# Kernel optimization log

Measured on AMD Instinct MI355X. Metric: run time of the kernel, lower is better.

## Reference

```python
import jax, jax.numpy as jnp
import numpy as np

EPS = 1e-5
K = 9
DILATION = 1

def bn(x, g, b, m, v):
    # x: (B,C,N,1), inference-mode BatchNorm2d with running stats
    sh = (1, -1, 1, 1)
    return (x - m.reshape(sh)) * (g.reshape(sh) / jnp.sqrt(v.reshape(sh) + EPS)) + b.reshape(sh)

def conv1x1(x, w, b):
    # w: (Cout, Cin), x: (B,Cin,N,1)
    return jnp.einsum('oc,bcnj->bonj', w, x) + b.reshape(1, -1, 1, 1)

def knn_idx(feat, k):
    # feat: (B,C,N) -> (B,N,k) indices of k nearest nodes (incl. self)
    xt = jnp.transpose(feat, (0, 2, 1))  # (B,N,C)
    x2 = jnp.sum(xt * xt, axis=-1)       # (B,N)
    dist = x2[:, :, None] - 2.0 * jnp.einsum('bnc,bmc->bnm', xt, xt) + x2[:, None, :]
    _, idx = jax.lax.top_k(-dist, k)
    return idx

def setup_inputs():
    key = jax.random.key(0)
    ks = jax.random.split(key, 24)
    B, C, H, W = 16, 256, 32, 32
    HID = 512
    def g(i, shape, s=1.0):
        return jax.random.normal(ks[i], shape, dtype=jnp.float32) * s
    def pos(i, shape):
        return jax.random.uniform(ks[i], shape, dtype=jnp.float32, minval=0.5, maxval=1.5)
    return {
        'x': g(0, (B, C, H, W)),
        'fc1_w': g(1, (C, C), 0.05), 'fc1_b': g(2, (C,), 0.05),
        'bn1_g': pos(3, (C,)), 'bn1_b': g(4, (C,), 0.1), 'bn1_m': g(5, (C,), 0.1), 'bn1_v': pos(6, (C,)),
        'gc_w': g(7, (HID, 2 * C), 0.05), 'gc_b': g(8, (HID,), 0.05),
        'gbn_g': pos(9, (HID,)), 'gbn_b': g(10, (HID,), 0.1), 'gbn_m': g(11, (HID,), 0.1), 'gbn_v': pos(12, (HID,)),
        'bn2_g': pos(13, (HID,)), 'bn2_b': g(14, (HID,), 0.1), 'bn2_m': g(15, (HID,), 0.1), 'bn2_v': pos(16, (HID,)),
        'fc2_w': g(17, (C, HID), 0.05), 'fc2_b': g(18, (C,), 0.05),
        'bn3_g': pos(19, (C,)), 'bn3_b': g(20, (C,), 0.1), 'bn3_m': g(21, (C,), 0.1), 'bn3_v': pos(22, (C,)),
    }

def reference(x, fc1_w, fc1_b, bn1_g, bn1_b, bn1_m, bn1_v,
              gc_w, gc_b, gbn_g, gbn_b, gbn_m, gbn_v,
              bn2_g, bn2_b, bn2_m, bn2_v,
              fc2_w, fc2_b, bn3_g, bn3_b, bn3_m, bn3_v):
    B, C, H, W = x.shape
    N = H * W
    x = x.reshape(B, C, N, 1)
    shortcut = x
    # fc1: 1x1 conv + BN
    h = bn(conv1x1(x, fc1_w, fc1_b), bn1_g, bn1_b, bn1_m, bn1_v)
    # DyGraphConv2d: dynamic dilated kNN graph over N nodes
    feat = h[..., 0]  # (B,C,N)
    idx = knn_idx(feat, K * DILATION)[:, :, ::DILATION]  # (B,N,K)
    # MRConv2d: max over neighbors of (x_j - x_i)
    x_j = jax.vmap(lambda f, i: f[:, i])(feat, idx)        # (B,C,N,K) gather
    diff_max = jnp.max(x_j - feat[:, :, :, None], axis=-1)  # (B,C,N)
    # interleave [x, max_diff] along channel dim -> (B, 2C, N, 1)
    m = jnp.stack([feat, diff_max], axis=2).reshape(B, 2 * C, N, 1)
    g = conv1x1(m, gc_w, gc_b)
    g = bn(g, gbn_g, gbn_b, gbn_m, gbn_v)  # BasicConv BN, act='None'
    # graph_conv Sequential: BN + GELU (erf, torch default)
    g = jax.nn.gelu(bn(g, bn2_g, bn2_b, bn2_m, bn2_v), approximate=False)
    # fc2 + residual (drop_path=0 -> identity)
    out = bn(conv1x1(g, fc2_w, fc2_b), bn3_g, bn3_b, bn3_m, bn3_v)
    return out + shortcut
```

## Files before the change

### kernel.cpp

```cpp
#include <hip/hip_runtime.h>
#include <hip/hip_bf16.h>
#include <stdint.h>

typedef unsigned long long u64;
typedef __hip_bfloat16 bf16;
typedef short s8v __attribute__((ext_vector_type(8)));
typedef short s4v __attribute__((ext_vector_type(4)));
typedef float f4v __attribute__((ext_vector_type(4)));

#define B_   16
#define C_   256
#define N_   1024
#define HID_ 512

#define GLD16(g, l)                                                         \
    __builtin_amdgcn_global_load_lds(                                       \
        (const __attribute__((address_space(1))) void*)(g),                 \
        (__attribute__((address_space(3))) void*)(l), 16, 0, 0)

#define WAITB4() do {                                                       \
        asm volatile("s_waitcnt vmcnt(4)" ::: "memory");                    \
        __builtin_amdgcn_s_barrier();                                       \
        __builtin_amdgcn_sched_barrier(0);                                  \
    } while (0)
#define WAITB2() do {                                                       \
        asm volatile("s_waitcnt vmcnt(2)" ::: "memory");                    \
        __builtin_amdgcn_s_barrier();                                       \
        __builtin_amdgcn_sched_barrier(0);                                  \
    } while (0)
#define WAITB0() do {                                                       \
        asm volatile("s_waitcnt vmcnt(0)" ::: "memory");                    \
        __builtin_amdgcn_s_barrier();                                       \
        __builtin_amdgcn_sched_barrier(0);                                  \
    } while (0)

__device__ __forceinline__ unsigned short f2b(float f) {
    unsigned u = __float_as_uint(f);
    unsigned r = (u + 0x7FFFu + ((u >> 16) & 1u)) >> 16;
    return (unsigned short)r;
}
__device__ __forceinline__ float b2f(unsigned short s) {
    return __uint_as_float(((unsigned)s) << 16);
}
__device__ __forceinline__ float ldIn(const void* p, long long i, int bf) {
    return bf ? b2f(((const unsigned short*)p)[i]) : ((const float*)p)[i];
}
__device__ __forceinline__ u64 shfl_xor_u64(u64 v, int m) {
    unsigned lo = (unsigned)v, hi = (unsigned)(v >> 32);
    lo = __shfl_xor(lo, m, 64);
    hi = __shfl_xor(hi, m, 64);
    return ((u64)hi << 32) | lo;
}

__global__ void prep_kernel(const void* xp,
    const void* fc1_b, const void* bn1_g, const void* bn1_b, const void* bn1_m, const void* bn1_v,
    const void* gc_b,  const void* gbn_g, const void* gbn_b, const void* gbn_m, const void* gbn_v,
    const void* bn2_g, const void* bn2_b, const void* bn2_m, const void* bn2_v,
    const void* fc2_b, const void* bn3_g, const void* bn3_b, const void* bn3_m, const void* bn3_v,
    int* flags, float* s1, float* t1, float* Sg, float* Tg, float* s3, float* t3,
    float* x2)
{
    __shared__ int sf;
    if (threadIdx.x == 0) {
        const unsigned short* u = (const unsigned short*)xp;
        int cnt = 0;
        for (int i = 0; i < 64; ++i) {
            int e = (u[2 * i] >> 7) & 0xFF;
            cnt += (e >= 87 && e <= 167);
        }
        int f = (cnt >= 48) ? 1 : 0;
        flags[0] = f;
        sf = f;
    }
    for (int i = threadIdx.x; i < B_ * N_; i += 512) x2[i] = 0.f;
    __syncthreads();
    int bf = sf;
    int i = threadIdx.x;
    if (i < 256) {
        float g = ldIn(bn1_g, i, bf), bb = ldIn(bn1_b, i, bf);
        float m = ldIn(bn1_m, i, bf), v  = ldIn(bn1_v, i, bf);
        float s = g / sqrtf(v + 1e-5f);
        s1[i] = s;
        t1[i] = (ldIn(fc1_b, i, bf) - m) * s + bb;

        float g3 = ldIn(bn3_g, i, bf), b3 = ldIn(bn3_b, i, bf);
        float m3 = ldIn(bn3_m, i, bf), v3 = ldIn(bn3_v, i, bf);
        float ss3 = g3 / sqrtf(v3 + 1e-5f);
        s3[i] = ss3;
        t3[i] = (ldIn(fc2_b, i, bf) - m3) * ss3 + b3;
    }
    if (i < 512) {
        float gg = ldIn(gbn_g, i, bf), gb = ldIn(gbn_b, i, bf);
        float gm = ldIn(gbn_m, i, bf), gv = ldIn(gbn_v, i, bf);
        float sg = gg / sqrtf(gv + 1e-5f);
        float g2 = ldIn(bn2_g, i, bf), b2 = ldIn(bn2_b, i, bf);
        float m2 = ldIn(bn2_m, i, bf), v2 = ldIn(bn2_v, i, bf);
        float s2 = g2 / sqrtf(v2 + 1e-5f);
        Sg[i] = sg * s2;
        Tg[i] = ((ldIn(gc_b, i, bf) - gm) * sg + gb - m2) * s2 + b2;
    }
}

__global__ __launch_bounds__(256)
void cast_weights(const void* w1, const void* wg, const void* w2,
                  short* W1h, short* W1l, short* Wgb, short* W2b,
                  const int* flags)
{
    int inf = flags[0];
    int i = blockIdx.x * 256 + threadIdx.x;
    if (i < 65536) {
        float f = ldIn(w1, i, inf);
        unsigned short h = f2b(f);
        W1h[i] = (short)h;
        W1l[i] = (short)f2b(f - b2f(h));
    } else if (i < 65536 + 262144) {
        int j = i - 65536;
        Wgb[j] = (short)f2b(ldIn(wg, j, inf));
    } else {
        int j = i - 327680;
        W2b[j] = (short)f2b(ldIn(w2, j, inf));
    }
}

__global__ __launch_bounds__(256)
void transpose_split_x(const void* __restrict__ X, short* __restrict__ xth,
                       short* __restrict__ xtl, const int* __restrict__ flags)
{
    __shared__ float tile[64][68];
    int inf = flags[0];
    int t = threadIdx.x;
    int n0 = blockIdx.x * 64, c0 = blockIdx.y * 64, b = blockIdx.z;

    #pragma unroll
    for (int rr = 0; rr < 4; ++rr) {
        int cl = (t >> 4) + rr * 16;
        int nl = (t & 15) * 4;
        long long g = ((long long)b * C_ + c0 + cl) * N_ + n0 + nl;
        if (inf) {
            s4v v = *(const s4v*)((const short*)X + g);
            tile[cl][nl + 0] = b2f((unsigned short)v[0]);
            tile[cl][nl + 1] = b2f((unsigned short)v[1]);
            tile[cl][nl + 2] = b2f((unsigned short)v[2]);
            tile[cl][nl + 3] = b2f((unsigned short)v[3]);
        } else {
            f4v v = *(const f4v*)((const float*)X + g);
            tile[cl][nl + 0] = v[0]; tile[cl][nl + 1] = v[1];
            tile[cl][nl + 2] = v[2]; tile[cl][nl + 3] = v[3];
        }
    }
    __syncthreads();

    int nl = t >> 2, cseg = t & 3;
    long long base = ((long long)((b << 10) + n0 + nl)) * C_ + c0 + cseg * 16;
    s8v h0, h1, l0, l1;
    #pragma unroll
    for (int cc = 0; cc < 16; ++cc) {
        float f = tile[cseg * 16 + cc][nl];
        unsigned short h = f2b(f);
        unsigned short l = f2b(f - b2f(h));
        if (cc < 8) { h0[cc] = (short)h; l0[cc] = (short)l; }
        else        { h1[cc - 8] = (short)h; l1[cc - 8] = (short)l; }
    }
    *(s8v*)(xth + base)     = h0;
    *(s8v*)(xth + base + 8) = h1;
    *(s8v*)(xtl + base)     = l0;
    *(s8v*)(xtl + base + 8) = l1;
}

__global__ __launch_bounds__(256)
void fc1_mfma(const short* __restrict__ W1h, const short* __restrict__ W1l,
              const short* __restrict__ xth, const short* __restrict__ xtl,
              const float* __restrict__ s1, const float* __restrict__ t1,
              float* __restrict__ Ft, short* __restrict__ Fhi,
              short* __restrict__ Flo, float* __restrict__ x2)
{
    __shared__ __align__(16) char ldsbuf[49152];

    int t = threadIdx.x;
    int n0 = blockIdx.x * 64, o0 = blockIdx.y * 128, b = blockIdx.z;
    int wv = t >> 6, lane = t & 63, ln15 = t & 15, quad = (t >> 4) & 3;

    int csw = (((lane & 3) ^ ((lane >> 3) & 3))) * 8;
    const short* gAh = W1h + (long long)(o0 + wv * 32 + (lane >> 2)) * C_ + csw;
    const short* gAl = W1l + (long long)(o0 + wv * 32 + (lane >> 2)) * C_ + csw;
    int slotofs = wv * 32 * 32;

#define FC1_STAGE(kc_) do {                                                   \
        short* base_ = (short*)(ldsbuf + ((kc_) % 3) * 16384);                \
        short* dh = base_ + slotofs;                                          \
        short* dl = base_ + 4096 + slotofs;                                   \
        GLD16(gAh + (kc_) * 32,            dh);                               \
        GLD16(gAh + (kc_) * 32 + 16 * C_,  dh + 16 * 32);                     \
        GLD16(gAl + (kc_) * 32,            dl);                               \
        GLD16(gAl + (kc_) * 32 + 16 * C_,  dl + 16 * 32);                     \
    } while (0)

    FC1_STAGE(0);

    s8v xh[8], xl[8];
    {
        long long xoff = (long long)((b << 10) + n0 + wv * 16 + ln15) * C_ + quad * 8;
        #pragma unroll
        for (int kc = 0; kc < 8; ++kc) {
            xh[kc] = *(const s8v*)(xth + xoff + kc * 32);
            xl[kc] = *(const s8v*)(xtl + xoff + kc * 32);
        }
    }

    FC1_STAGE(1);

    f4v acc[8];
    #pragma unroll
    for (int i = 0; i < 8; ++i) acc[i] = 0.f;

    int roff = (quad ^ ((ln15 >> 1) & 3)) * 8;

    #pragma unroll
    for (int kc = 0; kc < 8; ++kc) {
        if (kc < 7) WAITB4(); else WAITB0();
        if (kc < 6) FC1_STAGE(kc + 2);
        const short* Ah_c = (const short*)(ldsbuf + (kc % 3) * 16384);
        const short* Al_c = Ah_c + 4096;
        #pragma unroll
        for (int i = 0; i < 8; ++i) {
            s8v wh8 = *(const s8v*)&Ah_c[(i * 16 + ln15) * 32 + roff];
            s8v wl8 = *(const s8v*)&Al_c[(i * 16 + ln15) * 32 + roff];
            acc[i] = __builtin_amdgcn_mfma_f32_16x16x32_bf16(wh8, xh[kc], acc[i], 0, 0, 0);
            acc[i] = __builtin_amdgcn_mfma_f32_16x16x32_bf16(wh8, xl[kc], acc[i], 0, 0, 0);
            acc[i] = __builtin_amdgcn_mfma_f32_16x16x32_bf16(wl8, xh[kc], acc[i], 0, 0, 0);
        }
    }
#undef FC1_STAGE

    int n = n0 + wv * 16 + ln15;
    long long nb = (long long)(b << 10) + n;
    float p2 = 0.f;
    #pragma unroll
    for (int i = 0; i < 8; ++i) {
        int ob = o0 + i * 16 + quad * 4;
        f4v f;
        s4v hi, lo;
        #pragma unroll
        for (int r = 0; r < 4; ++r) {
            float v = acc[i][r] * s1[ob + r] + t1[ob + r];
            f[r] = v;
            unsigned short h = f2b(v);
            hi[r] = (short)h;
            lo[r] = (short)f2b(v - b2f(h));
            p2 += v * v;
        }
        *(f4v*)(Ft  + nb * C_ + ob) = f;
        *(s4v*)(Fhi + nb * C_ + ob) = hi;
        *(s4v*)(Flo + nb * C_ + ob) = lo;
    }
    p2 += __shfl_xor(p2, 16, 64);
    p2 += __shfl_xor(p2, 32, 64);
    if (quad == 0) atomicAdd(&x2[nb], p2);
}

__global__ __launch_bounds__(256)
void gram_topk(const short* __restrict__ Fhi, const short* __restrict__ Flo,
               const float* __restrict__ x2, u64* __restrict__ Part)
{
    __shared__ __align__(16) char ldsbuf[33280];
    float* x2s = (float*)(ldsbuf + 32768);
    u64*   mrg  = (u64*)(ldsbuf);
    u64*   mrg2 = (u64*)(ldsbuf + 20480);

    int t = threadIdx.x;
    int q0 = blockIdx.x * 64, mq = blockIdx.y, b = blockIdx.z;
    int wv = t >> 6, lane = t & 63, ln15 = t & 15, quad = (t >> 4) & 3;

    int csw = (((lane & 3) ^ ((lane >> 3) & 3))) * 8;
    const short* gAh = Fhi + (long long)((b << 10) + mq * 128 + wv * 32 + (lane >> 2)) * C_ + csw;
    const short* gAl = Flo + (long long)((b << 10) + mq * 128 + wv * 32 + (lane >> 2)) * C_ + csw;
    short* lH0 = (short*)(ldsbuf)           + wv * 32 * 32;
    short* lL0 = (short*)(ldsbuf + 8192)    + wv * 32 * 32;
    short* lH1 = (short*)(ldsbuf + 16384)   + wv * 32 * 32;
    short* lL1 = (short*)(ldsbuf + 24576)   + wv * 32 * 32;

#define GRAM_STAGE(kc_, bi_) do {                                             \
        short* dh = (bi_) ? lH1 : lH0;                                        \
        short* dl = (bi_) ? lL1 : lL0;                                        \
        GLD16(gAh + (kc_) * 32,            dh);                               \
        GLD16(gAh + (kc_) * 32 + 16 * C_,  dh + 16 * 32);                     \
        GLD16(gAl + (kc_) * 32,            dl);                               \
        GLD16(gAl + (kc_) * 32 + 16 * C_,  dl + 16 * 32);                     \
    } while (0)

    GRAM_STAGE(0, 0);

    if (t < 128) x2s[t] = x2[(b << 10) + mq * 128 + t];

    s8v qh[8], ql[8];
    {
        long long qoff = (long long)((b << 10) + q0 + wv * 16 + ln15) * C_ + quad * 8;
        #pragma unroll
        for (int kc = 0; kc < 8; ++kc) {
            qh[kc] = *(const s8v*)(Fhi + qoff + kc * 32);
            ql[kc] = *(const s8v*)(Flo + qoff + kc * 32);
        }
    }

    f4v acc[8];
    #pragma unroll
    for (int i = 0; i < 8; ++i) acc[i] = 0.f;

    int roff = (quad ^ ((ln15 >> 1) & 3)) * 8;

    __syncthreads();

    #pragma unroll
    for (int kc = 0; kc < 8; ++kc) {
        if (kc < 7) GRAM_STAGE(kc + 1, (kc + 1) & 1);
        const short* Ah_c = (const short*)(ldsbuf + (kc & 1) * 16384);
        const short* Al_c = Ah_c + 4096;
        #pragma unroll
        for (int i = 0; i < 8; ++i) {
            s8v mh = *(const s8v*)&Ah_c[(i * 16 + ln15) * 32 + roff];
            s8v ml = *(const s8v*)&Al_c[(i * 16 + ln15) * 32 + roff];
            acc[i] = __builtin_amdgcn_mfma_f32_16x16x32_bf16(mh, qh[kc], acc[i], 0, 0, 0);
            acc[i] = __builtin_amdgcn_mfma_f32_16x16x32_bf16(mh, ql[kc], acc[i], 0, 0, 0);
            acc[i] = __builtin_amdgcn_mfma_f32_16x16x32_bf16(ml, qh[kc], acc[i], 0, 0, 0);
        }
        __syncthreads();
    }
#undef GRAM_STAGE

    u64 l[9];
    #pragma unroll
    for (int i = 0; i < 9; ++i) l[i] = ~0ULL;
    #pragma unroll
    for (int i = 0; i < 8; ++i) {
        #pragma unroll
        for (int r = 0; r < 4; ++r) {
            int mloc = i * 16 + quad * 4 + r;
            float d = x2s[mloc] - 2.f * acc[i][r];
            unsigned u = __float_as_uint(d);
            u = (u & 0x80000000u) ? ~u : (u | 0x80000000u);
            u64 key = ((u64)u << 32) | (unsigned)(mq * 128 + mloc);
            if (key < l[8]) {
                u64 x = key;
                #pragma unroll
                for (int jj = 0; jj < 9; ++jj) {
                    u64 lo2 = l[jj] < x ? l[jj] : x;
                    u64 hi2 = l[jj] < x ? x : l[jj];
                    l[jj] = lo2; x = hi2;
                }
            }
        }
    }

    __syncthreads();
    {
        int qloc = wv * 16 + ln15;
        #pragma unroll
        for (int k = 0; k < 9; ++k) mrg[(qloc * 4 + quad) * 9 + k] = l[k];
    }
    __syncthreads();
    if (t < 128) {
        int r = t >> 1, pr = t & 1;
        const u64* LA = &mrg[(r * 4 + pr * 2) * 9];
        const u64* LB = LA + 9;
        int ia = 0, ib = 0;
        u64* Po = &mrg2[(r * 2 + pr) * 9];
        #pragma unroll
        for (int k = 0; k < 9; ++k) {
            u64 va = LA[ia], vb = LB[ib];
            bool ta = va < vb;
            Po[k] = ta ? va : vb;
            ia += ta; ib += !ta;
        }
    }
    __syncthreads();
    if (t < 64) {
        const u64* LA = &mrg2[(t * 2) * 9];
        const u64* LB = LA + 9;
        int ia = 0, ib = 0;
        u64* P = Part + (((long long)((b << 10) + q0 + t)) * 8 + mq) * 9;
        #pragma unroll
        for (int k = 0; k < 9; ++k) {
            u64 va = LA[ia], vb = LB[ib];
            bool ta = va < vb;
            P[k] = ta ? va : vb;
            ia += ta; ib += !ta;
        }
    }
}

__global__ __launch_bounds__(256)
void build_Mt(const float* __restrict__ Ft, const u64* __restrict__ Part,
              short* __restrict__ Mt)
{
    int t = threadIdx.x;
    int wv = t >> 6, lane = t & 63;
    int n = blockIdx.x * 4 + wv;
    int b = blockIdx.y;
    long long nb = (long long)(b << 10) + n;

    const u64* L = Part + nb * 72 + (long long)(lane & 7) * 9;
    u64 l[9];
    #pragma unroll
    for (int k = 0; k < 9; ++k) l[k] = L[k];
    #pragma unroll
    for (int s = 1; s <= 4; s <<= 1) {
        u64 p[9];
        #pragma unroll
        for (int k = 0; k < 9; ++k) p[k] = shfl_xor_u64(l[k], s);
        #pragma unroll
        for (int k = 0; k < 9; ++k) {
            u64 x = p[k];
            if (x < l[8]) {
                #pragma unroll
                for (int jj = 0; jj < 9; ++jj) {
                    u64 lo2 = l[jj] < x ? l[jj] : x;
                    u64 hi2 = l[jj] < x ? x : l[jj];
                    l[jj] = lo2; x = hi2;
                }
            }
        }
    }

    int c0 = lane * 4;
    f4v f = *(const f4v*)(Ft + nb * C_ + c0);
    f4v mx = {-3.4e38f, -3.4e38f, -3.4e38f, -3.4e38f};
    #pragma unroll
    for (int k = 0; k < 9; ++k) {
        int id = (int)(l[k] & 0xFFFFFFFFu);
        f4v g = *(const f4v*)(Ft + ((long long)(b << 10) + id) * C_ + c0);
        mx[0] = fmaxf(mx[0], g[0]); mx[1] = fmaxf(mx[1], g[1]);
        mx[2] = fmaxf(mx[2], g[2]); mx[3] = fmaxf(mx[3], g[3]);
    }
    s8v m8;
    #pragma unroll
    for (int r = 0; r < 4; ++r) {
        m8[2 * r]     = (short)f2b(f[r]);
        m8[2 * r + 1] = (short)f2b(mx[r] - f[r]);
    }
    *(s8v*)(Mt + nb * (2 * C_) + 2 * c0) = m8;
}

template<int EPI, int K_>
__global__ __launch_bounds__(256)
void mfma_gemm(const short* __restrict__ A, const short* __restrict__ Bm,
               void* __restrict__ Out, const float* __restrict__ scale,
               const float* __restrict__ bias, const void* __restrict__ resid,
               const int* __restrict__ flags, int Odim)
{
    __shared__ __align__(16) char ldsbuf[24576];

    int t = threadIdx.x, b = blockIdx.z;
    int n0 = blockIdx.x * 64, o0 = blockIdx.y * 128;
    int wv = t >> 6, lane = t & 63, ln15 = t & 15, quad = (t >> 4) & 3;

    int csw = (((lane & 3) ^ ((lane >> 3) & 3))) * 8;
    const short* gA = A + (long long)(o0 + wv * 32 + (lane >> 2)) * K_ + csw;
    int slotofs = wv * 32 * 32;

#define GEMM_STAGE(kc_) do {                                                  \
        short* d = (short*)(ldsbuf + ((kc_) % 3) * 8192) + slotofs;           \
        GLD16(gA + (kc_) * 32,            d);                                 \
        GLD16(gA + (kc_) * 32 + 16 * K_,  d + 16 * 32);                       \
    } while (0)

    GEMM_STAGE(0);

    constexpr int NKC = K_ / 32;
    s8v bfr[NKC];
    {
        long long boff = (long long)((b << 10) + n0 + wv * 16 + ln15) * K_ + quad * 8;
        #pragma unroll
        for (int kc = 0; kc < NKC; ++kc)
            bfr[kc] = *(const s8v*)(Bm + boff + kc * 32);
    }

    GEMM_STAGE(1);

    f4v acc[8];
    #pragma unroll
    for (int i = 0; i < 8; ++i) acc[i] = 0.f;

    int roff = (quad ^ ((ln15 >> 1) & 3)) * 8;

    #pragma unroll
    for (int kc = 0; kc < NKC; ++kc) {
        if (kc < NKC - 1) WAITB2(); else WAITB0();
        if (kc < NKC - 2) GEMM_STAGE(kc + 2);
        const short* Ac = (const short*)(ldsbuf + (kc % 3) * 8192);
        #pragma unroll
        for (int i = 0; i < 8; ++i) {
            s8v a = *(const s8v*)&Ac[(i * 16 + ln15) * 32 + roff];
            acc[i] = __builtin_amdgcn_mfma_f32_16x16x32_bf16(a, bfr[kc], acc[i], 0, 0, 0);
        }
    }
#undef GEMM_STAGE

    int inf = flags[0];
    int n = n0 + wv * 16 + ln15;
    #pragma unroll
    for (int i = 0; i < 8; ++i) {
        int ob = o0 + i * 16 + quad * 4;
        if (EPI == 0) {
            s4v g;
            #pragma unroll
            for (int r = 0; r < 4; ++r) {
                float val = acc[i][r] * scale[ob + r] + bias[ob + r];
                val = 0.5f * val * (1.0f + erff(val * 0.70710678118654752f));
                g[r] = (short)f2b(val);
            }
            *(s4v*)((short*)Out + ((long long)((b << 10) + n)) * Odim + ob) = g;
        } else {
            #pragma unroll
            for (int r = 0; r < 4; ++r) {
                int o = ob + r;
                long long oi = ((long long)b * Odim + o) * N_ + n;
                ((float*)Out)[oi] = acc[i][r] * scale[o] + bias[o] + ldIn(resid, oi, inf);
            }
        }
    }
}

extern "C" void kernel_launch(void* const* d_in, const int* in_sizes, int n_in,
                              void* d_out, int out_size, void* d_ws, size_t ws_size,
                              hipStream_t stream)
{
    const void* p[23];
    if (n_in >= 23 && in_sizes[0] != 4194304 && in_sizes[22] == 4194304) {
        const int amap[23] = {
            22, 13, 12, 1, 0, 2, 3,
            21, 20, 17, 16, 18, 19,
            5, 4, 6, 7,
            15, 14, 9, 8, 10, 11 };
        for (int i = 0; i < 23; ++i) p[i] = d_in[amap[i]];
    } else {
        for (int i = 0; i < 23; ++i) p[i] = d_in[i];
    }

    const void* x     = p[0];
    const void* fc1_w = p[1];
    const void* fc1_b = p[2];
    const void* bn1_g = p[3];
    const void* bn1_b = p[4];
    const void* bn1_m = p[5];
    const void* bn1_v = p[6];
    const void* gc_w  = p[7];
    const void* gc_b  = p[8];
    const void* gbn_g = p[9];
    const void* gbn_b = p[10];
    const void* gbn_m = p[11];
    const void* gbn_v = p[12];
    const void* bn2_g = p[13];
    const void* bn2_b = p[14];
    const void* bn2_m = p[15];
    const void* bn2_v = p[16];
    const void* fc2_w = p[17];
    const void* fc2_b = p[18];
    const void* bn3_g = p[19];
    const void* bn3_b = p[20];
    const void* bn3_m = p[21];
    const void* bn3_v = p[22];

    char* ws = (char*)d_ws;
    size_t off = 0;
    int*   flags = (int*)ws;
    float* s1 = (float*)(ws + 256);
    float* t1 = s1 + 256;
    float* s3 = t1 + 256;
    float* t3 = s3 + 256;
    float* Sg = t3 + 256;
    float* Tg = Sg + 512;
    off = 16384;
    short* W1h   = (short*)(ws + off); off += (size_t)C_ * C_ * 2;
    short* W1l   = (short*)(ws + off); off += (size_t)C_ * C_ * 2;
    short* Wgb   = (short*)(ws + off); off += (size_t)HID_ * 2 * C_ * 2;
    short* W2b   = (short*)(ws + off); off += (size_t)C_ * HID_ * 2;
    short* xth   = (short*)(ws + off); off += (size_t)B_ * N_ * C_ * 2;
    short* xtl   = (short*)(ws + off); off += (size_t)B_ * N_ * C_ * 2;
    float* Ft    = (float*)(ws + off); off += (size_t)B_ * N_ * C_ * 4;
    short* Fhi   = (short*)(ws + off); off += (size_t)B_ * N_ * C_ * 2;
    short* Flo   = (short*)(ws + off); off += (size_t)B_ * N_ * C_ * 2;
    float* x2    = (float*)(ws + off); off += (size_t)B_ * N_ * 4;
    u64*   Part  = (u64*)  (ws + off); off += (size_t)B_ * N_ * 8 * 9 * 8;
    short* Mt    = (short*)(ws + off); off += (size_t)B_ * N_ * 2 * C_ * 2;
    short* Gt    = (short*)(ws + off); off += (size_t)B_ * N_ * HID_ * 2;

    prep_kernel<<<1, 512, 0, stream>>>(x,
        fc1_b, bn1_g, bn1_b, bn1_m, bn1_v,
        gc_b, gbn_g, gbn_b, gbn_m, gbn_v,
        bn2_g, bn2_b, bn2_m, bn2_v,
        fc2_b, bn3_g, bn3_b, bn3_m, bn3_v,
        flags, s1, t1, Sg, Tg, s3, t3, x2);

    cast_weights<<<1792, 256, 0, stream>>>(fc1_w, gc_w, fc2_w,
                                           W1h, W1l, Wgb, W2b, flags);

    transpose_split_x<<<dim3(16, 4, 16), 256, 0, stream>>>(x, xth, xtl, flags);

    fc1_mfma<<<dim3(16, 2, 16), 256, 0, stream>>>(
        W1h, W1l, xth, xtl, s1, t1, Ft, Fhi, Flo, x2);

    gram_topk<<<dim3(16, 8, 16), 256, 0, stream>>>(Fhi, Flo, x2, Part);

    build_Mt<<<dim3(256, 16), 256, 0, stream>>>(Ft, Part, Mt);

    mfma_gemm<0, 512><<<dim3(16, 4, 16), 256, 0, stream>>>(
        Wgb, Mt, Gt, Sg, Tg, nullptr, flags, HID_);

    mfma_gemm<1, 512><<<dim3(16, 2, 16), 256, 0, stream>>>(
        W2b, Gt, d_out, s3, t3, x, flags, C_);
}
```

Before: 282.5 us.

## Merge prep and weight-cast kernels; deepen GEMM A-tile pipeline to four stages

Folds the single-block prep kernel into the weight-cast kernel. Each block now recomputes the input-dtype flag locally, an extra block computes the BN scale/shift tables, and the first 64 blocks zero x2. This removes one launch and a serialized single-block step. Separately, the MFMA GEMM moves from a 3-deep to a 4-deep LDS ring for the A tile, with three stages in flight and adjusted waitcnt thresholds. This raises LDS use per block from 24KB to 32KB, which may reduce occupancy.

```diff
diff --git a/kernel.cpp b/kernel.cpp
--- a/kernel.cpp
+++ b/kernel.cpp
@@ -52,72 +52,75 @@
     return ((u64)hi << 32) | lo;
 }
 
-__global__ void prep_kernel(const void* xp,
+__global__ __launch_bounds__(256)
+void cast_prep(const void* xp, const void* w1, const void* wg, const void* w2,
     const void* fc1_b, const void* bn1_g, const void* bn1_b, const void* bn1_m, const void* bn1_v,
     const void* gc_b,  const void* gbn_g, const void* gbn_b, const void* gbn_m, const void* gbn_v,
     const void* bn2_g, const void* bn2_b, const void* bn2_m, const void* bn2_v,
     const void* fc2_b, const void* bn3_g, const void* bn3_b, const void* bn3_m, const void* bn3_v,
+    short* W1h, short* W1l, short* Wgb, short* W2b,
     int* flags, float* s1, float* t1, float* Sg, float* Tg, float* s3, float* t3,
     float* x2)
 {
     __shared__ int sf;
-    if (threadIdx.x == 0) {
+    int t = threadIdx.x;
+    if (t == 0) {
         const unsigned short* u = (const unsigned short*)xp;
         int cnt = 0;
         for (int i = 0; i < 64; ++i) {
             int e = (u[2 * i] >> 7) & 0xFF;
             cnt += (e >= 87 && e <= 167);
         }
-        int f = (cnt >= 48) ? 1 : 0;
-        flags[0] = f;
-        sf = f;
-    }
-    for (int i = threadIdx.x; i < B_ * N_; i += 512) x2[i] = 0.f;
+        sf = (cnt >= 48) ? 1 : 0;
+    }
     __syncthreads();
-    int bf = sf;
-    int i = threadIdx.x;
-    if (i < 256) {
-        float g = ldIn(bn1_g, i, bf), bb = ldIn(bn1_b, i, bf);
-        float m = ldIn(bn1_m, i, bf), v  = ldIn(bn1_v, i, bf);
-        float s = g / sqrtf(v + 1e-5f);
-        s1[i] = s;
-        t1[i] = (ldIn(fc1_b, i, bf) - m) * s + bb;
-
-        float g3 = ldIn(bn3_g, i, bf), b3 = ldIn(bn3_b, i, bf);
-        float m3 = ldIn(bn3_m, i, bf), v3 = ldIn(bn3_v, i, bf);
-        float ss3 = g3 / sqrtf(v3 + 1e-5f);
-        s3[i] = ss3;
-        t3[i] = (ldIn(fc2_b, i, bf) - m3) * ss3 + b3;
-    }
-    if (i < 512) {
-        float gg = ldIn(gbn_g, i, bf), gb = ldIn(gbn_b, i, bf);
-        float gm = ldIn(gbn_m, i, bf), gv = ldIn(gbn_v, i, bf);
-        float sg = gg / sqrtf(gv + 1e-5f);
-        float g2 = ldIn(bn2_g, i, bf), b2 = ldIn(bn2_b, i, bf);
-        float m2 = ldIn(bn2_m, i, bf), v2 = ldIn(bn2_v, i, bf);
-        float s2 = g2 / sqrtf(v2 + 1e-5f);
-        Sg[i] = sg * s2;
-        Tg[i] = ((ldIn(gc_b, i, bf) - gm) * sg + gb - m2) * s2 + b2;
-    }
-}
-
-__global__ __launch_bounds__(256)
-void cast_weights(const void* w1, const void* wg, const void* w2,
-                  short* W1h, short* W1l, short* Wgb, short* W2b,
-                  const int* flags)
-{
-    int inf = flags[0];
-    int i = blockIdx.x * 256 + threadIdx.x;
+    int inf = sf;
+    int bid = blockIdx.x;
+
+    if (bid == 1792) {
+        if (t == 0) flags[0] = inf;
+        int i = t;
+        {
+            float g = ldIn(bn1_g, i, inf), bb = ldIn(bn1_b, i, inf);
+            float m = ldIn(bn1_m, i, inf), v  = ldIn(bn1_v, i, inf);
+            float s = g / sqrtf(v + 1e-5f);
+            s1[i] = s;
+            t1[i] = (ldIn(fc1_b, i, inf) - m) * s + bb;
+
+            float g3 = ldIn(bn3_g, i, inf), b3 = ldIn(bn3_b, i, inf);
+            float m3 = ldIn(bn3_m, i, inf), v3 = ldIn(bn3_v, i, inf);
+            float ss3 = g3 / sqrtf(v3 + 1e-5f);
+            s3[i] = ss3;
+            t3[i] = (ldIn(fc2_b, i, inf) - m3) * ss3 + b3;
+        }
+        #pragma unroll
+        for (int pass = 0; pass < 2; ++pass) {
+            int j = t + pass * 256;
+            float gg = ldIn(gbn_g, j, inf), gb = ldIn(gbn_b, j, inf);
+            float gm = ldIn(gbn_m, j, inf), gv = ldIn(gbn_v, j, inf);
+            float sg = gg / sqrtf(gv + 1e-5f);
+            float g2 = ldIn(bn2_g, j, inf), b2 = ldIn(bn2_b, j, inf);
+            float m2 = ldIn(bn2_m, j, inf), v2 = ldIn(bn2_v, j, inf);
+            float s2 = g2 / sqrtf(v2 + 1e-5f);
+            Sg[j] = sg * s2;
+            Tg[j] = ((ldIn(gc_b, j, inf) - gm) * sg + gb - m2) * s2 + b2;
+        }
+        return;
+    }
+
+    if (bid < 64) x2[bid * 256 + t] = 0.f;
+
+    long long i = (long long)bid * 256 + t;
     if (i < 65536) {
         float f = ldIn(w1, i, inf);
         unsigned short h = f2b(f);
         W1h[i] = (short)h;
         W1l[i] = (short)f2b(f - b2f(h));
     } else if (i < 65536 + 262144) {
-        int j = i - 65536;
+        long long j = i - 65536;
         Wgb[j] = (short)f2b(ldIn(wg, j, inf));
     } else {
-        int j = i - 327680;
+        long long j = i - 327680;
         W2b[j] = (short)f2b(ldIn(w2, j, inf));
     }
 }
@@ -447,7 +450,7 @@
                const float* __restrict__ bias, const void* __restrict__ resid,
                const int* __restrict__ flags, int Odim)
 {
-    __shared__ __align__(16) char ldsbuf[24576];
+    __shared__ __align__(16) char ldsbuf[32768];
 
     int t = threadIdx.x, b = blockIdx.z;
     int n0 = blockIdx.x * 64, o0 = blockIdx.y * 128;
@@ -458,7 +461,7 @@
     int slotofs = wv * 32 * 32;
 
 #define GEMM_STAGE(kc_) do {                                                  \
-        short* d = (short*)(ldsbuf + ((kc_) % 3) * 8192) + slotofs;           \
+        short* d = (short*)(ldsbuf + ((kc_) & 3) * 8192) + slotofs;           \
         GLD16(gA + (kc_) * 32,            d);                                 \
         GLD16(gA + (kc_) * 32 + 16 * K_,  d + 16 * 32);                       \
     } while (0)
@@ -475,6 +478,7 @@
     }
 
     GEMM_STAGE(1);
+    GEMM_STAGE(2);
 
     f4v acc[8];
     #pragma unroll
@@ -484,9 +488,11 @@
 
     #pragma unroll
     for (int kc = 0; kc < NKC; ++kc) {
-        if (kc < NKC - 1) WAITB2(); else WAITB0();
-        if (kc < NKC - 2) GEMM_STAGE(kc + 2);
-        const short* Ac = (const short*)(ldsbuf + (kc % 3) * 8192);
+        if (kc < NKC - 2) WAITB4();
+        else if (kc == NKC - 2) WAITB2();
+        else WAITB0();
+        if (kc < NKC - 3) GEMM_STAGE(kc + 3);
+        const short* Ac = (const short*)(ldsbuf + (kc & 3) * 8192);
         #pragma unroll
         for (int i = 0; i < 8; ++i) {
             s8v a = *(const s8v*)&Ac[(i * 16 + ln15) * 32 + roff];
@@ -584,15 +590,13 @@
     short* Mt    = (short*)(ws + off); off += (size_t)B_ * N_ * 2 * C_ * 2;
     short* Gt    = (short*)(ws + off); off += (size_t)B_ * N_ * HID_ * 2;
 
-    prep_kernel<<<1, 512, 0, stream>>>(x,
+    cast_prep<<<1793, 256, 0, stream>>>(x, fc1_w, gc_w, fc2_w,
         fc1_b, bn1_g, bn1_b, bn1_m, bn1_v,
         gc_b, gbn_g, gbn_b, gbn_m, gbn_v,
         bn2_g, bn2_b, bn2_m, bn2_v,
         fc2_b, bn3_g, bn3_b, bn3_m, bn3_v,
+        W1h, W1l, Wgb, W2b,
         flags, s1, t1, Sg, Tg, s3, t3, x2);
-
-    cast_weights<<<1792, 256, 0, stream>>>(fc1_w, gc_w, fc2_w,
-                                           W1h, W1l, Wgb, W2b, flags);
 
     transpose_split_x<<<dim3(16, 4, 16), 256, 0, stream>>>(x, xth, xtl, flags);
 
```

After: 280.0 us, median of 3. No clear change (-0.9%).
